# Kernel tuning notes

Measured on AMD Instinct MI355X. Metric: run time of the kernel, lower is better.

Reference implementation:

```python
import jax, jax.numpy as jnp
import numpy as np

N, C, H, D, K = 16384, 256, 8, 64, 8
HID, OUT, NE = 512, 64, 64
COMMIT, RADIUS, RHID = 0.25, 10.0, 16


def setup_inputs() -> dict:
    key = jax.random.key(0)
    ks = jax.random.split(key, 20)
    def w(k, shape, fan_in):
        return jax.random.normal(k, shape, jnp.float32) / np.sqrt(fan_in).astype(np.float32)
    return {
        'x': jax.random.normal(ks[0], (N, C), jnp.float32),
        'coors': jax.random.normal(ks[1], (N, 3), jnp.float32) * 3.0,
        'nbr_idx': jax.random.randint(ks[2], (N, K), 0, N, jnp.int32),
        'Wq': w(ks[3], (C, H * D), C),
        'Wk': w(ks[4], (C, H * D), C),
        'Wv': w(ks[5], (C, H * D), C),
        'w_gate': w(ks[6], (C, H), C),
        'Wr1': w(ks[7], (1, RHID), 1),
        'br1': jnp.zeros((RHID,), jnp.float32),
        'Wr2': w(ks[8], (RHID, H), RHID),
        'br2': jnp.zeros((H,), jnp.float32),
        'Wo': w(ks[9], (H * D + H, C), H * D + H),
        'alpha1': jnp.float32(0.5) * jnp.ones((), jnp.float32),
        'gamma1': jnp.ones((C,), jnp.float32),
        'beta1': jnp.zeros((C,), jnp.float32),
        'Wlin': w(ks[10], (C, HID), C),
        'blin': jnp.zeros((HID,), jnp.float32),
        'alpha2': jnp.float32(0.5) * jnp.ones((), jnp.float32),
        'gamma2': jnp.ones((HID + 20,), jnp.float32),
        'beta2': jnp.zeros((HID + 20,), jnp.float32),
        'Wout': w(ks[11], (HID + 20, OUT), HID + 20),
        'bout': jnp.zeros((OUT,), jnp.float32),
        'codebook': jax.random.normal(ks[12], (NE, OUT), jnp.float32),
    }


def reference(x, coors, Wq, Wk, Wv, w_gate, Wr1, br1, Wr2, br2, Wo,
              alpha1, gamma1, beta1, Wlin, blin, alpha2, gamma2, beta2,
              Wout, bout, codebook, nbr_idx):
    # ---- SE(3)-equivariant sparse-neighbor attention (heads=8, dim_head=64, K=8) ----
    q = (x @ Wq).reshape(N, H, D)
    xn = x[nbr_idx]                                  # [N,K,C] neighbor gather
    k = (xn @ Wk).reshape(N, K, H, D)
    v = (xn @ Wv).reshape(N, K, H, D)
    rel = coors[nbr_idx] - coors[:, None, :]         # [N,K,3]
    dist = jnp.sqrt(jnp.sum(rel * rel, -1) + 1e-8)   # [N,K]
    unit = rel / dist[..., None]
    radial = jax.nn.gelu(dist[..., None] @ Wr1 + br1) @ Wr2 + br2   # [N,K,H]
    logits = jnp.einsum('nhd,nkhd->nkh', q, k) / np.float32(np.sqrt(D)) + radial
    logits = jnp.where((dist <= RADIUS)[..., None], logits, jnp.float32(-1e9))
    attn = jax.nn.softmax(logits, axis=1)            # over K neighbors
    out0 = jnp.einsum('nkh,nkhd->nhd', attn, v).reshape(N, H * D)   # degree-0
    gate = xn @ w_gate                               # [N,K,H]
    vec = jnp.einsum('nkh,nkx->nhx', attn * gate, unit)             # degree-1 [N,H,3]
    vecnorm = jnp.sqrt(jnp.sum(vec * vec, -1) + 1e-8)               # invariant [N,H]
    se3_out = x + jnp.concatenate([out0, vecnorm], -1) @ Wo         # residual
    # ---- lin: DynamicTanh -> Linear -> GELU ----
    h = jnp.tanh(alpha1 * se3_out) * gamma1 + beta1
    h = jax.nn.gelu(h @ Wlin + blin)
    # ---- out_dense: concat 20-dim aa feats, DynamicTanh -> Linear -> GELU -> Tanh ----
    h2 = jnp.concatenate([h, x[:, :20]], -1)
    h2 = jnp.tanh(alpha2 * h2) * gamma2 + beta2
    z = jnp.tanh(jax.nn.gelu(h2 @ Wout + bout))      # [N,OUT]
    # ---- VQ-EMA: nearest codebook entry, commitment loss, straight-through ----
    d2 = (jnp.sum(z * z, -1, keepdims=True)
          - 2.0 * z @ codebook.T
          + jnp.sum(codebook * codebook, -1))
    idx = jnp.argmin(d2, axis=-1)
    zq = codebook[idx]
    vq_loss = COMMIT * jnp.mean((z - jax.lax.stop_gradient(zq)) ** 2)
    z_quantized = z + jax.lax.stop_gradient(zq - z)
    return z_quantized, vq_loss
```

## Files before the change

kernel.cpp:

```cpp
#include <hip/hip_runtime.h>
#include <hip/hip_bf16.h>
#include <stdint.h>

#define NPTS 16384
#define CDIM 256
#define HEADS 8
#define KNBR 8
#define HIDD 512
#define OUTD 64
#define NEMB 64
#define RHIDD 16

typedef _Float16 half8 __attribute__((ext_vector_type(8)));
typedef float f32x4 __attribute__((ext_vector_type(4)));

__device__ __forceinline__ float gelu_tanh(float v) {
    float v3 = v * v * v;
    return 0.5f * v * (1.0f + tanhf(0.79788456080286535588f * (v + 0.044715f * v3)));
}

__device__ __forceinline__ void gload16(const void* g, void* l) {
    __builtin_amdgcn_global_load_lds((const __attribute__((address_space(1))) void*)g,
                                     (__attribute__((address_space(3))) void*)l, 16, 0, 0);
}

__launch_bounds__(256)
__global__ void gemm_qkv(const _Float16* __restrict__ A2, const _Float16* __restrict__ B2,
                         float* __restrict__ QKV, float* __restrict__ G) {
    __shared__ __align__(16) char lds[32768];

    const int tid = threadIdx.x;
    const int l = tid & 63, w = tid >> 6;
    const int g = l >> 4, r = l & 15;
    const int wr = w >> 1, wc = w & 1;
    const int m0 = blockIdx.y * 128;
    const int n0 = blockIdx.x * 128;
    const int ldA = 512;
    const int srow = l >> 3;
    const int sl = (l & 7) ^ srow;
    const int scol = (sl & 3) * 8 + ((sl >= 4) ? 256 : 0);
    const int swz = (l & 7) << 4;
    const int aBase = (wr * 64 + r) * 128;
    const int bBase = 16384 + (wc * 64 + r) * 128;
    const int koh = (g << 4) ^ swz;
    const int kol = (64 | (g << 4)) ^ swz;

    f32x4 acc[4][4] = {};

    const _Float16* aS = A2 + (size_t)m0 * ldA + scol;
    const _Float16* bS = B2 + (size_t)n0 * ldA + scol;

    for (int t = 0; t < 8; ++t) {
        const int kk = t * 32;
        #pragma unroll
        for (int cc = 0; cc < 4; ++cc) {
            int ch = w * 4 + cc;
            int row = ch * 8 + srow;
            gload16(aS + (size_t)row * ldA + kk, lds + ch * 1024);
            gload16(bS + (size_t)row * ldA + kk, lds + 16384 + ch * 1024);
        }
        __syncthreads();
        half8 ah[4], bh[4], xf[4];
        #pragma unroll
        for (int i = 0; i < 4; ++i) ah[i] = *(const half8*)(lds + aBase + i * 2048 + koh);
        #pragma unroll
        for (int j = 0; j < 4; ++j) bh[j] = *(const half8*)(lds + bBase + j * 2048 + koh);
        #pragma unroll
        for (int i = 0; i < 4; ++i)
            #pragma unroll
            for (int j = 0; j < 4; ++j)
                acc[i][j] = __builtin_amdgcn_mfma_f32_16x16x32_f16(ah[i], bh[j], acc[i][j], 0, 0, 0);
        #pragma unroll
        for (int j = 0; j < 4; ++j) xf[j] = *(const half8*)(lds + bBase + j * 2048 + kol);
        #pragma unroll
        for (int i = 0; i < 4; ++i)
            #pragma unroll
            for (int j = 0; j < 4; ++j)
                acc[i][j] = __builtin_amdgcn_mfma_f32_16x16x32_f16(ah[i], xf[j], acc[i][j], 0, 0, 0);
        #pragma unroll
        for (int i = 0; i < 4; ++i) xf[i] = *(const half8*)(lds + aBase + i * 2048 + kol);
        #pragma unroll
        for (int i = 0; i < 4; ++i)
            #pragma unroll
            for (int j = 0; j < 4; ++j)
                acc[i][j] = __builtin_amdgcn_mfma_f32_16x16x32_f16(xf[i], bh[j], acc[i][j], 0, 0, 0);
        __syncthreads();
    }

    #pragma unroll
    for (int i = 0; i < 4; ++i) {
        #pragma unroll
        for (int j = 0; j < 4; ++j) {
            const int gcol = n0 + wc * 64 + j * 16 + r;
            #pragma unroll
            for (int q = 0; q < 4; ++q) {
                const int row = m0 + wr * 64 + i * 16 + g * 4 + q;
                float v = acc[i][j][q];
                if (gcol < 1536) {
                    QKV[(size_t)row * 1536 + gcol] = v;
                } else if (gcol < 1544) {
                    G[(size_t)row * 8 + (gcol - 1536)] = v;
                }
            }
        }
    }
}

template <int EPI>
__launch_bounds__(256)
__global__ void gemm_tail64(const _Float16* __restrict__ A2, const _Float16* __restrict__ B2,
                            int Kpad, int KT, void* __restrict__ Cout,
                            const float* __restrict__ bias,
                            const float* __restrict__ res,
                            const float* __restrict__ alphap,
                            const float* __restrict__ gamma,
                            const float* __restrict__ beta,
                            const float* __restrict__ a2p,
                            const float* __restrict__ g2,
                            const float* __restrict__ b2,
                            void* __restrict__ aux) {
    __shared__ __align__(16) char lds[49152];

    const int tid = threadIdx.x;
    const int l = tid & 63, w = tid >> 6;
    const int g = l >> 4, r = l & 15;
    const int m0 = blockIdx.y * 64;
    const int n0 = blockIdx.x * 128;
    const int ldA = 2 * Kpad;
    const int srow = l >> 3;
    const int sl = (l & 7) ^ srow;
    const int scol = (sl & 3) * 8 + ((sl >= 4) ? Kpad : 0);
    const int swz = (l & 7) << 4;
    const int koh = (g << 4) ^ swz;
    const int kol = (64 | (g << 4)) ^ swz;

    f32x4 acc[4][2] = {};

    const _Float16* aS = A2 + (size_t)m0 * ldA + scol;
    const _Float16* bS = B2 + (size_t)n0 * ldA + scol;

    auto stage = [&](int buf, int t) {
        const int kk = t * 32;
        char* d = lds + buf * 24576;
        #pragma unroll
        for (int cc = 0; cc < 2; ++cc) {
            int ch = w * 2 + cc;
            gload16(aS + (size_t)(ch * 8 + srow) * ldA + kk, d + ch * 1024);
        }
        #pragma unroll
        for (int cc = 0; cc < 4; ++cc) {
            int ch = w * 4 + cc;
            gload16(bS + (size_t)(ch * 8 + srow) * ldA + kk, d + 8192 + ch * 1024);
        }
    };

    stage(0, 0);
    for (int t = 0; t < KT; ++t) {
        const int cur = t & 1;
        if (t + 1 < KT) {
            stage(cur ^ 1, t + 1);
            asm volatile("s_waitcnt vmcnt(6)" ::: "memory");
        } else {
            asm volatile("s_waitcnt vmcnt(0)" ::: "memory");
        }
        __builtin_amdgcn_s_barrier();
        __builtin_amdgcn_sched_barrier(0);
        const char* Lb = lds + cur * 24576;
        half8 ah[4], bh[2], xf[4];
        #pragma unroll
        for (int i = 0; i < 4; ++i) ah[i] = *(const half8*)(Lb + (i * 16 + r) * 128 + koh);
        #pragma unroll
        for (int j = 0; j < 2; ++j) bh[j] = *(const half8*)(Lb + 8192 + (w * 32 + j * 16 + r) * 128 + koh);
        #pragma unroll
        for (int i = 0; i < 4; ++i)
            #pragma unroll
            for (int j = 0; j < 2; ++j)
                acc[i][j] = __builtin_amdgcn_mfma_f32_16x16x32_f16(ah[i], bh[j], acc[i][j], 0, 0, 0);
        #pragma unroll
        for (int j = 0; j < 2; ++j) xf[j] = *(const half8*)(Lb + 8192 + (w * 32 + j * 16 + r) * 128 + kol);
        #pragma unroll
        for (int i = 0; i < 4; ++i)
            #pragma unroll
            for (int j = 0; j < 2; ++j)
                acc[i][j] = __builtin_amdgcn_mfma_f32_16x16x32_f16(ah[i], xf[j], acc[i][j], 0, 0, 0);
        #pragma unroll
        for (int i = 0; i < 4; ++i) xf[i] = *(const half8*)(Lb + (i * 16 + r) * 128 + kol);
        #pragma unroll
        for (int i = 0; i < 4; ++i)
            #pragma unroll
            for (int j = 0; j < 2; ++j)
                acc[i][j] = __builtin_amdgcn_mfma_f32_16x16x32_f16(xf[i], bh[j], acc[i][j], 0, 0, 0);
        __builtin_amdgcn_s_barrier();
    }

    const float alp = alphap[0];
    #pragma unroll
    for (int i = 0; i < 4; ++i) {
        #pragma unroll
        for (int j = 0; j < 2; ++j) {
            const int gcol = n0 + w * 32 + j * 16 + r;
            #pragma unroll
            for (int q = 0; q < 4; ++q) {
                const int row = m0 + i * 16 + g * 4 + q;
                float v = acc[i][j][q];
                if (EPI == 1) {
                    v += res[(size_t)row * CDIM + gcol];
                    v = tanhf(alp * v) * gamma[gcol] + beta[gcol];
                    _Float16 hi = (_Float16)v;
                    _Float16 lo = (_Float16)(v - (float)hi);
                    _Float16* H = (_Float16*)Cout;
                    H[(size_t)row * 512 + gcol] = hi;
                    H[(size_t)row * 512 + 256 + gcol] = lo;
                    if (gcol < 64) {
                        int tc = 512 + gcol;
                        float tv = 0.f;
                        if (gcol < 20)
                            tv = tanhf(a2p[0] * res[(size_t)row * CDIM + gcol]) * g2[tc] + b2[tc];
                        _Float16 thi = (_Float16)tv;
                        _Float16 tlo = (_Float16)(tv - (float)thi);
                        _Float16* T = (_Float16*)aux;
                        T[(size_t)row * 1152 + tc] = thi;
                        T[(size_t)row * 1152 + 576 + tc] = tlo;
                    }
                } else {
                    v = gelu_tanh(v + bias[gcol]);
                    v = tanhf(alp * v) * gamma[gcol] + beta[gcol];
                    _Float16 hi = (_Float16)v;
                    _Float16 lo = (_Float16)(v - (float)hi);
                    _Float16* H = (_Float16*)Cout;
                    H[(size_t)row * 1152 + gcol] = hi;
                    H[(size_t)row * 1152 + 576 + gcol] = lo;
                }
            }
        }
    }
}

__launch_bounds__(256)
__global__ void gemm_out_vq(const _Float16* __restrict__ A2, const _Float16* __restrict__ B2,
                            const float* __restrict__ bout, const float* __restrict__ cb,
                            float* __restrict__ outZ, float* __restrict__ outLoss) {
    __shared__ __align__(16) char lds[34816];
    __shared__ float psum[64];
    float* zL  = (float*)lds;
    float* cbL = (float*)(lds + 17408);

    const int tid = threadIdx.x;
    const int l = tid & 63, w = tid >> 6;
    const int g = l >> 4, r = l & 15;
    const int wr = w >> 1, wc = w & 1;
    const int m0 = blockIdx.x * 64;
    const int Kpad = 576;
    const int ldA = 1152;
    const int srow = l >> 3;
    const int sl = (l & 7) ^ srow;
    const int scol = (sl & 3) * 8 + ((sl >= 4) ? Kpad : 0);
    const int swz = (l & 7) << 4;
    const int aBase = (wr * 32 + r) * 128;
    const int bBase = 8192 + (wc * 32 + r) * 128;
    const int koh = (g << 4) ^ swz;
    const int kol = (64 | (g << 4)) ^ swz;

    f32x4 acc[2][2] = {};

    const _Float16* aS = A2 + (size_t)m0 * ldA + scol;
    const _Float16* bS = B2 + scol;

    auto stage = [&](int buf, int t) {
        const int kk = t * 32;
        char* d0 = lds + buf * 16384;
        #pragma unroll
        for (int cc = 0; cc < 2; ++cc) {
            int ch = w * 2 + cc;
            int row = ch * 8 + srow;
            gload16(aS + (size_t)row * ldA + kk, d0 + ch * 1024);
            gload16(bS + (size_t)row * ldA + kk, d0 + 8192 + ch * 1024);
        }
    };

    stage(0, 0);
    for (int t = 0; t < 18; ++t) {
        const int cur = t & 1;
        if (t + 1 < 18) {
            stage(cur ^ 1, t + 1);
            asm volatile("s_waitcnt vmcnt(4)" ::: "memory");
        } else {
            asm volatile("s_waitcnt vmcnt(0)" ::: "memory");
        }
        __builtin_amdgcn_s_barrier();
        __builtin_amdgcn_sched_barrier(0);
        const char* Lb = lds + cur * 16384;
        half8 ah[2], bh[2], xf[2];
        #pragma unroll
        for (int i = 0; i < 2; ++i) ah[i] = *(const half8*)(Lb + aBase + i * 2048 + koh);
        #pragma unroll
        for (int j = 0; j < 2; ++j) bh[j] = *(const half8*)(Lb + bBase + j * 2048 + koh);
        #pragma unroll
        for (int i = 0; i < 2; ++i)
            #pragma unroll
            for (int j = 0; j < 2; ++j)
                acc[i][j] = __builtin_amdgcn_mfma_f32_16x16x32_f16(ah[i], bh[j], acc[i][j], 0, 0, 0);
        #pragma unroll
        for (int j = 0; j < 2; ++j) xf[j] = *(const half8*)(Lb + bBase + j * 2048 + kol);
        #pragma unroll
        for (int i = 0; i < 2; ++i)
            #pragma unroll
            for (int j = 0; j < 2; ++j)
                acc[i][j] = __builtin_amdgcn_mfma_f32_16x16x32_f16(ah[i], xf[j], acc[i][j], 0, 0, 0);
        #pragma unroll
        for (int i = 0; i < 2; ++i) xf[i] = *(const half8*)(Lb + aBase + i * 2048 + kol);
        #pragma unroll
        for (int i = 0; i < 2; ++i)
            #pragma unroll
            for (int j = 0; j < 2; ++j)
                acc[i][j] = __builtin_amdgcn_mfma_f32_16x16x32_f16(xf[i], bh[j], acc[i][j], 0, 0, 0);
        __builtin_amdgcn_s_barrier();
    }

    #pragma unroll
    for (int i = 0; i < 2; ++i) {
        #pragma unroll
        for (int j = 0; j < 2; ++j) {
            int col = wc * 32 + j * 16 + r;
            #pragma unroll
            for (int q = 0; q < 4; ++q) {
                int rl = wr * 32 + i * 16 + g * 4 + q;
                zL[rl * 68 + col] = tanhf(gelu_tanh(acc[i][j][q] + bout[col]));
            }
        }
    }
    for (int i = tid; i < NEMB * OUTD / 4; i += 256) {
        float4 v = ((const float4*)cb)[i];
        int e = (i * 4) >> 6, c0 = (i * 4) & 63;
        cbL[e * 68 + c0 + 0] = v.x; cbL[e * 68 + c0 + 1] = v.y;
        cbL[e * 68 + c0 + 2] = v.z; cbL[e * 68 + c0 + 3] = v.w;
    }
    __syncthreads();
    if (tid < 64) {
        float cc = 0.f;
        #pragma unroll
        for (int d = 0; d < 64; ++d) { float cv = cbL[tid * 68 + d]; cc += cv * cv; }
        cbL[tid * 68 + 64] = cc;
    }
    __syncthreads();

    const int row = tid >> 2, part = tid & 3;
    float best = 1e30f;
    int bidx = 0;
    for (int e = part * 16; e < part * 16 + 16; ++e) {
        float dot = 0.f;
        #pragma unroll
        for (int d = 0; d < 64; ++d) dot += zL[row * 68 + d] * cbL[e * 68 + d];
        float sc = cbL[e * 68 + 64] - 2.f * dot;
        if (sc < best) { best = sc; bidx = e; }
    }
    #pragma unroll
    for (int m = 1; m <= 2; m <<= 1) {
        float ob = __shfl_xor(best, m, 64);
        int oi = __shfl_xor(bidx, m, 64);
        if (ob < best || (ob == best && oi < bidx)) { best = ob; bidx = oi; }
    }
    const int grow = m0 + row;
    float lsum = 0.f;
    #pragma unroll
    for (int u = 0; u < 16; ++u) {
        float cv = cbL[bidx * 68 + part * 16 + u];
        outZ[(size_t)grow * 64 + part * 16 + u] = cv;
        float df = zL[row * 68 + part * 16 + u] - cv;
        lsum += df * df;
    }
    lsum += __shfl_xor(lsum, 1, 64);
    lsum += __shfl_xor(lsum, 2, 64);
    if (part == 0) psum[row] = lsum;
    __syncthreads();
    if (tid < 64) {
        float v = psum[tid];
        #pragma unroll
        for (int m = 1; m < 64; m <<= 1) v += __shfl_xor(v, m, 64);
        if (tid == 0)
            atomicAdd(outLoss, v * (0.25f / ((float)NPTS * (float)OUTD)));
    }
}

#define R0SZ (NPTS * CDIM)
#define S1 (1664 * 256)
#define S2 (256 * 576)
#define S3 (512 * 256)
#define S4 (64 * 576)
__global__ void prep(const float* __restrict__ x,
                     const float* __restrict__ Wq, const float* __restrict__ Wk,
                     const float* __restrict__ Wv, const float* __restrict__ w_gate,
                     const float* __restrict__ Wo, const float* __restrict__ Wlin,
                     const float* __restrict__ Wout,
                     _Float16* __restrict__ x2, _Float16* __restrict__ wqkv2,
                     _Float16* __restrict__ wo2, _Float16* __restrict__ wlin2,
                     _Float16* __restrict__ wout2, float* __restrict__ outLoss) {
    if (blockIdx.x == 0 && threadIdx.x == 0) *outLoss = 0.f;
    for (int idx = blockIdx.x * 256 + threadIdx.x; idx < R0SZ + S1 + S2 + S3 + S4;
         idx += gridDim.x * 256) {
        float v; _Float16* dst; size_t o0, o1;
        if (idx < R0SZ) {
            int n = idx >> 8, cc = idx & 255;
            v = x[idx];
            dst = x2; o0 = (size_t)n * 512 + cc; o1 = o0 + 256;
        } else if (idx < R0SZ + S1) {
            int t = idx - R0SZ;
            int j = t >> 8, k = t & 255;
            if (j < 1536) {
                int jm = j & 511;
                const float* W = (j < 512) ? Wq : (j < 1024) ? Wk : Wv;
                v = W[(size_t)k * 512 + jm];
            } else if (j < 1544) {
                v = w_gate[(size_t)k * 8 + (j - 1536)];
            } else {
                v = 0.f;
            }
            dst = wqkv2; o0 = (size_t)j * 512 + k; o1 = o0 + 256;
        } else if (idx < R0SZ + S1 + S2) {
            int t = idx - R0SZ - S1;
            int j = t / 576, k = t - j * 576;
            v = (k < 520) ? Wo[(size_t)k * 256 + j] : 0.f;
            dst = wo2; o0 = (size_t)j * 1152 + k; o1 = o0 + 576;
        } else if (idx < R0SZ + S1 + S2 + S3) {
            int t = idx - R0SZ - S1 - S2;
            int j = t >> 8, k = t & 255;
            v = Wlin[(size_t)k * 512 + j];
            dst = wlin2; o0 = (size_t)j * 512 + k; o1 = o0 + 256;
        } else {
            int t = idx - R0SZ - S1 - S2 - S3;
            int j = t / 576, k = t - j * 576;
            v = (k < 532) ? Wout[(size_t)k * 64 + j] : 0.f;
            dst = wout2; o0 = (size_t)j * 1152 + k; o1 = o0 + 576;
        }
        _Float16 hi = (_Float16)v, lo = (_Float16)(v - (float)hi);
        dst[o0] = hi; dst[o1] = lo;
    }
}

__launch_bounds__(256)
__global__ void attn_kernel(const float* __restrict__ QKV, const float* __restrict__ G,
                            const float* __restrict__ coors, const int* __restrict__ nbr,
                            const float* __restrict__ Wr1, const float* __restrict__ br1,
                            const float* __restrict__ Wr2, const float* __restrict__ br2,
                            _Float16* __restrict__ att2) {
    __shared__ float unitL[4][8][3];
    __shared__ float distL[4][8];
    __shared__ float radH[4][8][16];

    const int tid = threadIdx.x;
    const int w = tid >> 6;
    const int lane = tid & 63;
    const int n = blockIdx.x * 4 + w;
    const int h = lane >> 3;
    const int c = lane & 7;

    int jreg[KNBR];
    #pragma unroll
    for (int k = 0; k < KNBR; ++k) jreg[k] = nbr[(size_t)n * KNBR + k];

    if (lane < KNBR) {
        int jj = jreg[lane];
        float rx = coors[(size_t)jj * 3 + 0] - coors[(size_t)n * 3 + 0];
        float ry = coors[(size_t)jj * 3 + 1] - coors[(size_t)n * 3 + 1];
        float rz = coors[(size_t)jj * 3 + 2] - coors[(size_t)n * 3 + 2];
        float d = sqrtf(rx * rx + ry * ry + rz * rz + 1e-8f);
        float inv = 1.0f / d;
        distL[w][lane] = d;
        unitL[w][lane][0] = rx * inv;
        unitL[w][lane][1] = ry * inv;
        unitL[w][lane][2] = rz * inv;
    }

    const float4* qp = (const float4*)(QKV + (size_t)n * 1536 + lane * 8);
    float4 q0 = qp[0], q1 = qp[1];
    float p[KNBR];
    #pragma unroll
    for (int k = 0; k < KNBR; ++k) {
        const float4* kp = (const float4*)(QKV + (size_t)jreg[k] * 1536 + 512 + lane * 8);
        float4 k0 = kp[0], k1 = kp[1];
        p[k] = q0.x * k0.x + q0.y * k0.y + q0.z * k0.z + q0.w * k0.w
             + q1.x * k1.x + q1.y * k1.y + q1.z * k1.z + q1.w * k1.w;
    }
    #pragma unroll
    for (int m = 1; m <= 4; m <<= 1) {
        #pragma unroll
        for (int k = 0; k < KNBR; ++k) p[k] += __shfl_xor(p[k], m, 64);
    }
    __syncthreads();

    #pragma unroll
    for (int rr = 0; rr < 2; ++rr) {
        int idx = lane + rr * 64;
        int k = idx >> 4, i = idx & 15;
        float hv = distL[w][k] * Wr1[i] + br1[i];
        radH[w][k][i] = gelu_tanh(hv);
    }
    __syncthreads();

    float lg[KNBR];
    float b2v = br2[h];
    #pragma unroll
    for (int k = 0; k < KNBR; ++k) {
        float rad = b2v;
        #pragma unroll
        for (int i = 0; i < RHIDD; ++i) rad += radH[w][k][i] * Wr2[i * HEADS + h];
        lg[k] = p[k] * 0.125f + rad;
        if (!(distL[w][k] <= 10.0f)) lg[k] = -1e9f;
    }
    float mx = lg[0];
    #pragma unroll
    for (int k = 1; k < KNBR; ++k) mx = fmaxf(mx, lg[k]);
    float a[KNBR];
    float s = 0.f;
    #pragma unroll
    for (int k = 0; k < KNBR; ++k) { a[k] = expf(lg[k] - mx); s += a[k]; }
    float is = 1.0f / s;
    #pragma unroll
    for (int k = 0; k < KNBR; ++k) a[k] *= is;

    float vx = 0.f, vy = 0.f, vz = 0.f;
    #pragma unroll
    for (int k = 0; k < KNBR; ++k) {
        float gg = G[(size_t)jreg[k] * HEADS + h];
        float ag = a[k] * gg;
        vx += ag * unitL[w][k][0];
        vy += ag * unitL[w][k][1];
        vz += ag * unitL[w][k][2];
    }
    float vn = sqrtf(vx * vx + vy * vy + vz * vz + 1e-8f);

    float4 o0 = {0.f, 0.f, 0.f, 0.f}, o1 = {0.f, 0.f, 0.f, 0.f};
    #pragma unroll
    for (int k = 0; k < KNBR; ++k) {
        const float4* vp = (const float4*)(QKV + (size_t)jreg[k] * 1536 + 1024 + lane * 8);
        float4 v0 = vp[0], v1 = vp[1];
        float ak = a[k];
        o0.x += ak * v0.x; o0.y += ak * v0.y; o0.z += ak * v0.z; o0.w += ak * v0.w;
        o1.x += ak * v1.x; o1.y += ak * v1.y; o1.z += ak * v1.z; o1.w += ak * v1.w;
    }

    float ov[8] = {o0.x, o0.y, o0.z, o0.w, o1.x, o1.y, o1.z, o1.w};
    half8 hi8, lo8;
    #pragma unroll
    for (int t = 0; t < 8; ++t) {
        _Float16 hi = (_Float16)ov[t];
        hi8[t] = hi;
        lo8[t] = (_Float16)(ov[t] - (float)hi);
    }
    *(half8*)(att2 + (size_t)n * 1152 + lane * 8) = hi8;
    *(half8*)(att2 + (size_t)n * 1152 + 576 + lane * 8) = lo8;
    if (c == 0) {
        _Float16 hi = (_Float16)vn, lo = (_Float16)(vn - (float)hi);
        att2[(size_t)n * 1152 + 512 + h] = hi;
        att2[(size_t)n * 1152 + 576 + 512 + h] = lo;
    }
    if (lane < 56) {
        att2[(size_t)n * 1152 + 520 + lane] = (_Float16)0.f;
        att2[(size_t)n * 1152 + 1096 + lane] = (_Float16)0.f;
    }
}

extern "C" void kernel_launch(void* const* d_in, const int* in_sizes, int n_in,
                              void* d_out, int out_size, void* d_ws, size_t ws_size,
                              hipStream_t stream) {
    const float* x      = (const float*)d_in[0];
    const float* coors  = (const float*)d_in[1];
    const int*   nbr    = (const int*)  d_in[2];
    const float* Wq     = (const float*)d_in[3];
    const float* Wk     = (const float*)d_in[4];
    const float* Wv     = (const float*)d_in[5];
    const float* w_gate = (const float*)d_in[6];
    const float* Wr1    = (const float*)d_in[7];
    const float* br1    = (const float*)d_in[8];
    const float* Wr2    = (const float*)d_in[9];
    const float* br2    = (const float*)d_in[10];
    const float* Wo     = (const float*)d_in[11];
    const float* alpha1 = (const float*)d_in[12];
    const float* gamma1 = (const float*)d_in[13];
    const float* beta1  = (const float*)d_in[14];
    const float* Wlin   = (const float*)d_in[15];
    const float* blin   = (const float*)d_in[16];
    const float* alpha2 = (const float*)d_in[17];
    const float* gamma2 = (const float*)d_in[18];
    const float* beta2  = (const float*)d_in[19];
    const float* Wout   = (const float*)d_in[20];
    const float* bout   = (const float*)d_in[21];
    const float* cb     = (const float*)d_in[22];

    char* wsb = (char*)d_ws;
    float*    QKV   = (float*)   (wsb + 0);
    _Float16* att2  = (_Float16*)(wsb + 100663296);
    _Float16* x2    = (_Float16*)(wsb + 138412032);
    _Float16* wqkv2 = (_Float16*)(wsb + 155189248);
    _Float16* wo2   = (_Float16*)(wsb + 156893184);
    _Float16* wlin2 = (_Float16*)(wsb + 157483008);
    _Float16* wout2 = (_Float16*)(wsb + 158007296);
    float*    G     = (float*)   (wsb + 158154752);
    _Float16* h1s   = (_Float16*)(wsb + 0);
    _Float16* h2s   = (_Float16*)(wsb + 20299776);

    float* outZ    = (float*)d_out;
    float* outLoss = outZ + (size_t)NPTS * OUTD;

    dim3 blk(256);

    prep<<<dim3(2048), blk, 0, stream>>>(x, Wq, Wk, Wv, w_gate, Wo, Wlin, Wout,
                                         x2, wqkv2, wo2, wlin2, wout2, outLoss);
    gemm_qkv<<<dim3(13, 128), blk, 0, stream>>>(x2, wqkv2, QKV, G);
    attn_kernel<<<dim3(NPTS / 4), blk, 0, stream>>>(QKV, G, coors, nbr, Wr1, br1, Wr2, br2, att2);
    gemm_tail64<1><<<dim3(2, 256), blk, 0, stream>>>(att2, wo2, 576, 18, h1s,
        nullptr, x, alpha1, gamma1, beta1, alpha2, gamma2, beta2, h2s);
    gemm_tail64<2><<<dim3(4, 256), blk, 0, stream>>>(h1s, wlin2, 256, 8, h2s,
        blin, nullptr, alpha2, gamma2, beta2, nullptr, nullptr, nullptr, nullptr);
    gemm_out_vq<<<dim3(256), blk, 0, stream>>>(h2s, wout2, bout, cb, outZ, outLoss);
}
```

Baseline: 376.9 us.

## Remap GEMM workgroups across XCDs and halve VQ tile rows for more blocks

```diff
diff --git a/kernel.cpp b/kernel.cpp
--- a/kernel.cpp
+++ b/kernel.cpp
@@ -33,8 +33,10 @@
     const int l = tid & 63, w = tid >> 6;
     const int g = l >> 4, r = l & 15;
     const int wr = w >> 1, wc = w & 1;
-    const int m0 = blockIdx.y * 128;
-    const int n0 = blockIdx.x * 128;
+    const int orig = blockIdx.y * 13 + blockIdx.x;
+    const int wgid = (orig & 7) * 208 + (orig >> 3);
+    const int m0 = (wgid / 13) * 128;
+    const int n0 = (wgid % 13) * 128;
     const int ldA = 512;
     const int srow = l >> 3;
     const int sl = (l & 7) ^ srow;
@@ -124,8 +126,11 @@
     const int tid = threadIdx.x;
     const int l = tid & 63, w = tid >> 6;
     const int g = l >> 4, r = l & 15;
-    const int m0 = blockIdx.y * 64;
-    const int n0 = blockIdx.x * 128;
+    const int nwg = gridDim.x * gridDim.y;
+    const int orig = blockIdx.y * gridDim.x + blockIdx.x;
+    const int wgid = (orig & 7) * (nwg >> 3) + (orig >> 3);
+    const int m0 = (wgid / gridDim.x) * 64;
+    const int n0 = (wgid % gridDim.x) * 128;
     const int ldA = 2 * Kpad;
     const int srow = l >> 3;
     const int sl = (l & 7) ^ srow;
@@ -240,41 +245,40 @@
 __global__ void gemm_out_vq(const _Float16* __restrict__ A2, const _Float16* __restrict__ B2,
                             const float* __restrict__ bout, const float* __restrict__ cb,
                             float* __restrict__ outZ, float* __restrict__ outLoss) {
-    __shared__ __align__(16) char lds[34816];
-    __shared__ float psum[64];
+    __shared__ __align__(16) char lds[26624];
+    __shared__ float psum[32];
     float* zL  = (float*)lds;
-    float* cbL = (float*)(lds + 17408);
+    float* cbL = (float*)(lds + 8704);
 
     const int tid = threadIdx.x;
     const int l = tid & 63, w = tid >> 6;
     const int g = l >> 4, r = l & 15;
     const int wr = w >> 1, wc = w & 1;
-    const int m0 = blockIdx.x * 64;
+    const int m0 = blockIdx.x * 32;
     const int Kpad = 576;
     const int ldA = 1152;
     const int srow = l >> 3;
     const int sl = (l & 7) ^ srow;
     const int scol = (sl & 3) * 8 + ((sl >= 4) ? Kpad : 0);
     const int swz = (l & 7) << 4;
-    const int aBase = (wr * 32 + r) * 128;
-    const int bBase = 8192 + (wc * 32 + r) * 128;
+    const int aBase = (wr * 16 + r) * 128;
+    const int bBase = 4096 + (wc * 32 + r) * 128;
     const int koh = (g << 4) ^ swz;
     const int kol = (64 | (g << 4)) ^ swz;
 
-    f32x4 acc[2][2] = {};
+    f32x4 acc[2] = {};
 
     const _Float16* aS = A2 + (size_t)m0 * ldA + scol;
     const _Float16* bS = B2 + scol;
 
     auto stage = [&](int buf, int t) {
         const int kk = t * 32;
-        char* d0 = lds + buf * 16384;
+        char* d0 = lds + buf * 12288;
+        gload16(aS + (size_t)(w * 8 + srow) * ldA + kk, d0 + w * 1024);
         #pragma unroll
         for (int cc = 0; cc < 2; ++cc) {
             int ch = w * 2 + cc;
-            int row = ch * 8 + srow;
-            gload16(aS + (size_t)row * ldA + kk, d0 + ch * 1024);
-            gload16(bS + (size_t)row * ldA + kk, d0 + 8192 + ch * 1024);
+            gload16(bS + (size_t)(ch * 8 + srow) * ldA + kk, d0 + 4096 + ch * 1024);
         }
     };
 
@@ -283,50 +287,36 @@
         const int cur = t & 1;
         if (t + 1 < 18) {
             stage(cur ^ 1, t + 1);
-            asm volatile("s_waitcnt vmcnt(4)" ::: "memory");
+            asm volatile("s_waitcnt vmcnt(3)" ::: "memory");
         } else {
             asm volatile("s_waitcnt vmcnt(0)" ::: "memory");
         }
         __builtin_amdgcn_s_barrier();
         __builtin_amdgcn_sched_barrier(0);
-        const char* Lb = lds + cur * 16384;
-        half8 ah[2], bh[2], xf[2];
-        #pragma unroll
-        for (int i = 0; i < 2; ++i) ah[i] = *(const half8*)(Lb + aBase + i * 2048 + koh);
-        #pragma unroll
-        for (int j = 0; j < 2; ++j) bh[j] = *(const half8*)(Lb + bBase + j * 2048 + koh);
-        #pragma unroll
-        for (int i = 0; i < 2; ++i)
-            #pragma unroll
-            for (int j = 0; j < 2; ++j)
-                acc[i][j] = __builtin_amdgcn_mfma_f32_16x16x32_f16(ah[i], bh[j], acc[i][j], 0, 0, 0);
-        #pragma unroll
-        for (int j = 0; j < 2; ++j) xf[j] = *(const half8*)(Lb + bBase + j * 2048 + kol);
-        #pragma unroll
-        for (int i = 0; i < 2; ++i)
-            #pragma unroll
-            for (int j = 0; j < 2; ++j)
-                acc[i][j] = __builtin_amdgcn_mfma_f32_16x16x32_f16(ah[i], xf[j], acc[i][j], 0, 0, 0);
-        #pragma unroll
-        for (int i = 0; i < 2; ++i) xf[i] = *(const half8*)(Lb + aBase + i * 2048 + kol);
-        #pragma unroll
-        for (int i = 0; i < 2; ++i)
-            #pragma unroll
-            for (int j = 0; j < 2; ++j)
-                acc[i][j] = __builtin_amdgcn_mfma_f32_16x16x32_f16(xf[i], bh[j], acc[i][j], 0, 0, 0);
+        const char* Lb = lds + cur * 12288;
+        half8 ah, al, bh[2], xf[2];
+        ah = *(const half8*)(Lb + aBase + koh);
+        bh[0] = *(const half8*)(Lb + bBase + koh);
+        bh[1] = *(const half8*)(Lb + bBase + 2048 + koh);
+        acc[0] = __builtin_amdgcn_mfma_f32_16x16x32_f16(ah, bh[0], acc[0], 0, 0, 0);
+        acc[1] = __builtin_amdgcn_mfma_f32_16x16x32_f16(ah, bh[1], acc[1], 0, 0, 0);
+        xf[0] = *(const half8*)(Lb + bBase + kol);
+        xf[1] = *(const half8*)(Lb + bBase + 2048 + kol);
+        acc[0] = __builtin_amdgcn_mfma_f32_16x16x32_f16(ah, xf[0], acc[0], 0, 0, 0);
+        acc[1] = __builtin_amdgcn_mfma_f32_16x16x32_f16(ah, xf[1], acc[1], 0, 0, 0);
+        al = *(const half8*)(Lb + aBase + kol);
+        acc[0] = __builtin_amdgcn_mfma_f32_16x16x32_f16(al, bh[0], acc[0], 0, 0, 0);
+        acc[1] = __builtin_amdgcn_mfma_f32_16x16x32_f16(al, bh[1], acc[1], 0, 0, 0);
         __builtin_amdgcn_s_barrier();
     }
 
     #pragma unroll
-    for (int i = 0; i < 2; ++i) {
-        #pragma unroll
-        for (int j = 0; j < 2; ++j) {
-            int col = wc * 32 + j * 16 + r;
-            #pragma unroll
-            for (int q = 0; q < 4; ++q) {
-                int rl = wr * 32 + i * 16 + g * 4 + q;
-                zL[rl * 68 + col] = tanhf(gelu_tanh(acc[i][j][q] + bout[col]));
-            }
+    for (int j = 0; j < 2; ++j) {
+        int col = wc * 32 + j * 16 + r;
+        #pragma unroll
+        for (int q = 0; q < 4; ++q) {
+            int rl = wr * 16 + g * 4 + q;
+            zL[rl * 68 + col] = tanhf(gelu_tanh(acc[j][q] + bout[col]));
         }
     }
     for (int i = tid; i < NEMB * OUTD / 4; i += 256) {
@@ -344,10 +334,10 @@
     }
     __syncthreads();
 
-    const int row = tid >> 2, part = tid & 3;
+    const int row = tid >> 3, part = tid & 7;
     float best = 1e30f;
     int bidx = 0;
-    for (int e = part * 16; e < part * 16 + 16; ++e) {
+    for (int e = part * 8; e < part * 8 + 8; ++e) {
         float dot = 0.f;
         #pragma unroll
         for (int d = 0; d < 64; ++d) dot += zL[row * 68 + d] * cbL[e * 68 + d];
@@ -355,28 +345,29 @@
         if (sc < best) { best = sc; bidx = e; }
     }
     #pragma unroll
-    for (int m = 1; m <= 2; m <<= 1) {
+    for (int m = 1; m <= 4; m <<= 1) {
         float ob = __shfl_xor(best, m, 64);
         int oi = __shfl_xor(bidx, m, 64);
         if (ob < best || (ob == best && oi < bidx)) { best = ob; bidx = oi; }
     }
-    const int grow = m0 + row;
     float lsum = 0.f;
     #pragma unroll
-    for (int u = 0; u < 16; ++u) {
-        float cv = cbL[bidx * 68 + part * 16 + u];
-        outZ[(size_t)grow * 64 + part * 16 + u] = cv;
-        float df = zL[row * 68 + part * 16 + u] - cv;
+    for (int u = 0; u < 8; ++u) {
+        const int col = part * 8 + u;
+        float cv = cbL[bidx * 68 + col];
+        outZ[(size_t)(m0 + row) * 64 + col] = cv;
+        float df = zL[row * 68 + col] - cv;
         lsum += df * df;
     }
     lsum += __shfl_xor(lsum, 1, 64);
     lsum += __shfl_xor(lsum, 2, 64);
+    lsum += __shfl_xor(lsum, 4, 64);
     if (part == 0) psum[row] = lsum;
     __syncthreads();
-    if (tid < 64) {
+    if (tid < 32) {
         float v = psum[tid];
         #pragma unroll
-        for (int m = 1; m < 64; m <<= 1) v += __shfl_xor(v, m, 64);
+        for (int m = 1; m < 32; m <<= 1) v += __shfl_xor(v, m, 64);
         if (tid == 0)
             atomicAdd(outLoss, v * (0.25f / ((float)NPTS * (float)OUTD)));
     }
@@ -612,5 +603,5 @@
         nullptr, x, alpha1, gamma1, beta1, alpha2, gamma2, beta2, h2s);
     gemm_tail64<2><<<dim3(4, 256), blk, 0, stream>>>(h1s, wlin2, 256, 8, h2s,
         blin, nullptr, alpha2, gamma2, beta2, nullptr, nullptr, nullptr, nullptr);
-    gemm_out_vq<<<dim3(256), blk, 0, stream>>>(h2s, wout2, bout, cb, outZ, outLoss);
-}
+    gemm_out_vq<<<dim3(512), blk, 0, stream>>>(h2s, wout2, bout, cb, outZ, outLoss);
+}
```

Measured after the change: 360.4 us (median of 2 runs). 1.05x faster.
